# Kernel optimization log

Measured on AMD Instinct MI355X. Metric: run time of the kernel, lower is better.

The kernel has to match this reference:

```python
import jax, jax.numpy as jnp
import numpy as np

N_NODES = 50000
N_EDGES = 500000
D = 128
BN_EPS = 1e-5


def setup_inputs() -> dict:
    key = jax.random.key(0)
    ks = jax.random.split(key, 6)
    x = jax.random.normal(ks[0], (N_NODES, D), dtype=jnp.float32)
    edge_attr = jax.random.normal(ks[1], (N_EDGES, D), dtype=jnp.float32)
    edge_source = jax.random.randint(ks[2], (N_EDGES,), 0, N_NODES, dtype=jnp.int32)
    edge_target = jax.random.randint(ks[3], (N_EDGES,), 0, N_NODES, dtype=jnp.int32)
    # Linear weights stored as [in, out] = [3*D, D]; scaled like torch default init
    scale = 1.0 / np.sqrt(3 * D)
    Wf = jax.random.normal(ks[4], (3 * D, D), dtype=jnp.float32) * scale
    Ws = jax.random.normal(ks[5], (3 * D, D), dtype=jnp.float32) * scale
    bf = jnp.zeros((D,), dtype=jnp.float32)
    bs = jnp.zeros((D,), dtype=jnp.float32)
    gamma = jnp.ones((D,), dtype=jnp.float32)
    beta = jnp.zeros((D,), dtype=jnp.float32)
    return {"x": x, "edge_attr": edge_attr, "edge_source": edge_source,
            "edge_target": edge_target, "Wf": Wf, "bf": bf, "Ws": Ws, "bs": bs,
            "gamma": gamma, "beta": beta}


def reference(x, edge_attr, edge_source, edge_target, Wf, bf, Ws, bs, gamma, beta):
    # gather + concat: z is [E, 3*D]
    z = jnp.concatenate([x[edge_source], x[edge_target], edge_attr], axis=-1)
    # gated edge messages: sigmoid(linear_f(z)) * softplus(linear_s(z))  [E, D]
    msg = jax.nn.sigmoid(z @ Wf + bf) * jax.nn.softplus(z @ Ws + bs)
    # scatter-sum back to source nodes  [N, D]
    agg = jax.ops.segment_sum(msg, edge_source, num_segments=N_NODES)
    # BatchNorm1d (training mode: batch stats, biased variance)
    mean = jnp.mean(agg, axis=0)
    var = jnp.var(agg, axis=0)
    agg_bn = (agg - mean) * jax.lax.rsqrt(var + BN_EPS) * gamma + beta
    return jax.nn.softplus(x + agg_bn)
```

## Files before the change

### kernel.cpp

```cpp
#include <hip/hip_runtime.h>
#include <math.h>
#include <stdint.h>

#define N_NODES 50000
#define N_EDGES 500000
#define D 128
#define BE 128
#define NKT 6
#define WROW 72
#define WSLAB (256 * WROW)
#define MROW 136
#define LOG2E 1.4426950408889634f
#define LN2   0.6931471805599453f

typedef __attribute__((ext_vector_type(8))) short bf16x8;
typedef __attribute__((ext_vector_type(4))) float floatx4;

__device__ __forceinline__ float fast_sigmoid(float v) {
    return __builtin_amdgcn_rcpf(1.0f + __builtin_amdgcn_exp2f(-v * LOG2E));
}
__device__ __forceinline__ float fast_softplus(float v) {
    float t = __builtin_amdgcn_exp2f(-fabsf(v) * LOG2E);
    return fmaxf(v, 0.0f) + __builtin_amdgcn_logf(1.0f + t) * LN2;
}
__device__ __forceinline__ uint32_t pack_bf16(float a, float b) {
    union { float f; uint32_t u; } ca, cb; ca.f = a; cb.f = b;
    return __builtin_amdgcn_perm(cb.u + 0x8000u, ca.u + 0x8000u, 0x07060302);
}
__device__ __forceinline__ unsigned short f2bf(float f) {
    union { float f; uint32_t u; } c; c.f = f;
    return (unsigned short)((c.u + 0x8000u) >> 16);
}

__global__ __launch_bounds__(256) void wt_prepass(
    const float* __restrict__ Wf, const float* __restrict__ Ws,
    unsigned short* __restrict__ Wt)
{
    const int kt = blockIdx.x >> 3;
    const int i  = blockIdx.x & 7;
    const int n  = threadIdx.x;
    const float* src = (n < 128) ? (Wf + n) : (Ws + (n - 128));
    const int k0 = kt * 64 + i * 8;
    uint32_t u[4];
#pragma unroll
    for (int j = 0; j < 4; j++) {
        float a = src[(size_t)(k0 + 2 * j) * D];
        float b = src[(size_t)(k0 + 2 * j + 1) * D];
        u[j] = pack_bf16(a, b);
    }
    uint4 v; v.x = u[0]; v.y = u[1]; v.z = u[2]; v.w = u[3];
    *(uint4*)(Wt + (size_t)(kt * 256 + n) * WROW + i * 8) = v;
}

__global__ __launch_bounds__(512, 2) void edge_msg_mfma(
    const float* __restrict__ x, const float* __restrict__ edge_attr,
    const int* __restrict__ esrc, const int* __restrict__ etgt,
    const unsigned short* __restrict__ Wt,
    const float* __restrict__ bfp, const float* __restrict__ bsp,
    float* __restrict__ agg, unsigned short* __restrict__ msgs,
    int* __restrict__ cnt, int mode)
{
    __shared__ unsigned short sW[2 * WSLAB];
    __shared__ unsigned short sZ[BE * WROW];
    __shared__ int sSrc[BE];
    __shared__ int sTgt[BE];

    const int tid  = threadIdx.x;
    const int lane = tid & 63;
    const int w    = tid >> 6;
    const int wc   = w & 3;
    const int wr   = w >> 2;
    const int e0   = blockIdx.x * BE;

    if (tid < BE) {
        sSrc[tid] = (e0 + tid < N_EDGES) ? esrc[e0 + tid] : 0;
    } else if (tid < 2 * BE) {
        int m = tid - BE;
        sTgt[m] = (e0 + m < N_EDGES) ? etgt[e0 + m] : 0;
    }
    __syncthreads();

    floatx4 acc[4][4];
#pragma unroll
    for (int mt = 0; mt < 4; mt++)
#pragma unroll
        for (int nt = 0; nt < 4; nt++) {
            floatx4 z = {0.f, 0.f, 0.f, 0.f};
            acc[mt][nt] = z;
        }

    const int zm = tid >> 2;
    const int zk = (tid & 3) * 16;

    float4 zr0, zr1, zr2, zr3;

    auto issue_w = [&](int kt, int slab) {
        const char* gbase = (const char*)Wt + (size_t)kt * 36864 + lane * 16;
        char* lbase = (char*)sW + slab * 36864;
#pragma unroll
        for (int i = 0; i < 5; i++) {
            int c = w + i * 8;
            if (c < 36) {
                __builtin_amdgcn_global_load_lds(
                    (const __attribute__((address_space(1))) void*)(gbase + c * 1024),
                    (__attribute__((address_space(3))) void*)(lbase + c * 1024),
                    16, 0, 0);
            }
        }
    };
    auto issue_z = [&](int kt) {
        const float* zsrc;
        int half = (kt & 1) * 64;
        if (kt < 2)      zsrc = x + (size_t)sSrc[zm] * D + half;
        else if (kt < 4) zsrc = x + (size_t)sTgt[zm] * D + half;
        else {
            int eg = e0 + zm;
            zsrc = edge_attr + (size_t)(eg < N_EDGES ? eg : 0) * D + half;
        }
        zr0 = *(const float4*)(zsrc + zk);
        zr1 = *(const float4*)(zsrc + zk + 4);
        zr2 = *(const float4*)(zsrc + zk + 8);
        zr3 = *(const float4*)(zsrc + zk + 12);
    };

    issue_w(0, 0);
    issue_z(0);

#pragma unroll 1
    for (int kt = 0; kt < NKT; kt++) {
        {
            uint4 lo, hi;
            lo.x = pack_bf16(zr0.x, zr0.y); lo.y = pack_bf16(zr0.z, zr0.w);
            lo.z = pack_bf16(zr1.x, zr1.y); lo.w = pack_bf16(zr1.z, zr1.w);
            hi.x = pack_bf16(zr2.x, zr2.y); hi.y = pack_bf16(zr2.z, zr2.w);
            hi.z = pack_bf16(zr3.x, zr3.y); hi.w = pack_bf16(zr3.z, zr3.w);
            uint32_t* dz = (uint32_t*)(sZ + (size_t)zm * WROW) + (zk >> 1);
            *(uint4*)(dz)     = lo;
            *(uint4*)(dz + 4) = hi;
        }
        __syncthreads();

        if (kt + 1 < NKT) {
            issue_w(kt + 1, (kt + 1) & 1);
            issue_z(kt + 1);
        }

        const unsigned short* sWb = sW + (kt & 1) * WSLAB;
#pragma unroll
        for (int ks = 0; ks < 2; ks++) {
            const int kb = ks * 32 + (lane >> 4) * 8;
            bf16x8 afr[4];
#pragma unroll
            for (int mt = 0; mt < 4; mt++)
                afr[mt] = *(const bf16x8*)(sZ + (wr * 64 + mt * 16 + (lane & 15)) * WROW + kb);
            bf16x8 bfr[4];
#pragma unroll
            for (int nt = 0; nt < 4; nt++) {
                int n = (nt < 2) ? (wc * 32 + nt * 16 + (lane & 15))
                                 : (128 + wc * 32 + (nt - 2) * 16 + (lane & 15));
                bfr[nt] = *(const bf16x8*)(sWb + n * WROW + kb);
            }
#pragma unroll
            for (int mt = 0; mt < 4; mt++)
#pragma unroll
                for (int nt = 0; nt < 4; nt++)
                    acc[mt][nt] = __builtin_amdgcn_mfma_f32_16x16x32_bf16(
                        afr[mt], bfr[nt], acc[mt][nt], 0, 0, 0);
        }
        __builtin_amdgcn_s_barrier();
    }

    if (mode) {
        unsigned short* sM = sW;
#pragma unroll
        for (int nt = 0; nt < 2; nt++) {
            const int col = wc * 32 + nt * 16 + (lane & 15);
            const float bF = bfp[col];
            const float bS = bsp[col];
#pragma unroll
            for (int mt = 0; mt < 4; mt++) {
#pragma unroll
                for (int r = 0; r < 4; r++) {
                    int mm = wr * 64 + mt * 16 + (lane >> 4) * 4 + r;
                    float f = acc[mt][nt][r] + bF;
                    float s = acc[mt][nt + 2][r] + bS;
                    sM[mm * MROW + col] = f2bf(fast_sigmoid(f) * fast_softplus(s));
                }
            }
        }
        __syncthreads();
        {
            const int r = tid >> 2;
            const int c = tid & 3;
            if (e0 + r < N_EDGES) {
                const uint4* sp = (const uint4*)(sM + r * MROW + c * 32);
                uint4 v0 = sp[0], v1 = sp[1], v2 = sp[2], v3 = sp[3];
                uint4* dp = (uint4*)(msgs + (size_t)(e0 + r) * D + c * 32);
                dp[0] = v0; dp[1] = v1; dp[2] = v2; dp[3] = v3;
            }
        }
        if (tid < BE && e0 + tid < N_EDGES) atomicAdd(&cnt[sSrc[tid]], 1);
    } else {
#pragma unroll
        for (int nt = 0; nt < 2; nt++) {
            const int col = wc * 32 + nt * 16 + (lane & 15);
            const float bF = bfp[col];
            const float bS = bsp[col];
#pragma unroll
            for (int mt = 0; mt < 4; mt++) {
#pragma unroll
                for (int r = 0; r < 4; r++) {
                    int mm = wr * 64 + mt * 16 + (lane >> 4) * 4 + r;
                    int eg = e0 + mm;
                    if (eg >= N_EDGES) continue;
                    float f = acc[mt][nt][r] + bF;
                    float s = acc[mt][nt + 2][r] + bS;
                    atomicAdd(agg + (size_t)sSrc[mm] * D + col,
                              fast_sigmoid(f) * fast_softplus(s));
                }
            }
        }
    }
}

__global__ __launch_bounds__(1024) void scan1_kernel(
    const int* __restrict__ cnt, int* __restrict__ ofs, int* __restrict__ bsum)
{
    __shared__ int sh[1024];
    const int t = threadIdx.x;
    const int n = blockIdx.x * 1024 + t;
    int c = (n < N_NODES) ? cnt[n] : 0;
    sh[t] = c;
    __syncthreads();
    for (int off = 1; off < 1024; off <<= 1) {
        int v = (t >= off) ? sh[t - off] : 0;
        __syncthreads();
        sh[t] += v;
        __syncthreads();
    }
    if (n < N_NODES) ofs[n] = sh[t] - c;
    if (t == 1023) bsum[blockIdx.x] = sh[1023];
}

__global__ __launch_bounds__(64) void scan2_kernel(int* __restrict__ bsum)
{
    if (threadIdx.x == 0) {
        int v[49];
#pragma unroll
        for (int i = 0; i < 49; i++) v[i] = bsum[i];
        int run = 0;
#pragma unroll
        for (int i = 0; i < 49; i++) { bsum[i] = run; run += v[i]; }
    }
}

__global__ __launch_bounds__(512) void fill_kernel(
    const int* __restrict__ esrc, int* __restrict__ ofs,
    const int* __restrict__ bsum, int* __restrict__ eidx)
{
    int e = blockIdx.x * 512 + threadIdx.x;
    if (e < N_EDGES) {
        int s = esrc[e];
        int slot = atomicAdd(&ofs[s], 1) + bsum[s >> 10];
        eidx[slot] = e;
    }
}

__global__ __launch_bounds__(256) void gather_kernel(
    const unsigned short* __restrict__ msgs, const int* __restrict__ eidx,
    const int* __restrict__ cnt, const int* __restrict__ ofs,
    const int* __restrict__ bsum, float* __restrict__ agg)
{
    __shared__ float red[2][64][2];
    const int tid  = threadIdx.x;
    const int lane = tid & 63;
    const int w2   = (tid >> 6) & 1;
    const int h    = tid >> 7;
    const int n    = blockIdx.x * 2 + h;
    const int deg  = cnt[n];
    const int base = bsum[n >> 10] + ofs[n] - deg;
    float a0 = 0.0f, a1 = 0.0f;
    for (int j = w2; j < deg; j += 2) {
        int id = eidx[base + j];
        uint32_t p = *(const uint32_t*)(msgs + (size_t)id * D + 2 * lane);
        union { uint32_t u; float f; } c0, c1;
        c0.u = p << 16;
        c1.u = p & 0xFFFF0000u;
        a0 += c0.f; a1 += c1.f;
    }
    if (w2 == 1) { red[h][lane][0] = a0; red[h][lane][1] = a1; }
    __syncthreads();
    if (w2 == 0) {
        a0 += red[h][lane][0];
        a1 += red[h][lane][1];
        float2 o; o.x = a0; o.y = a1;
        *(float2*)(agg + (size_t)n * D + 2 * lane) = o;
    }
}

#define STATS_BLOCKS 128
__global__ __launch_bounds__(256) void bn_stats_kernel(
    const float* __restrict__ agg, float* __restrict__ stats)
{
    __shared__ float4 redS[256];
    __shared__ float4 redQ[256];
    const int c4 = threadIdx.x & 31;
    const int rg = threadIdx.x >> 5;
    const int rows = (N_NODES + STATS_BLOCKS - 1) / STATS_BLOCKS;
    const int r0 = blockIdx.x * rows;
    const int r1 = min(r0 + rows, N_NODES);
    const float4* a4 = (const float4*)agg;

    float4 s = {0, 0, 0, 0}, q = {0, 0, 0, 0};
    for (int r = r0 + rg; r < r1; r += 8) {
        float4 v = a4[(size_t)r * 32 + c4];
        s.x += v.x; s.y += v.y; s.z += v.z; s.w += v.w;
        q.x += v.x * v.x; q.y += v.y * v.y; q.z += v.z * v.z; q.w += v.w * v.w;
    }
    redS[threadIdx.x] = s;
    redQ[threadIdx.x] = q;
    __syncthreads();
    if (rg == 0) {
#pragma unroll
        for (int j = 1; j < 8; j++) {
            float4 ts = redS[c4 + j * 32], tq = redQ[c4 + j * 32];
            s.x += ts.x; s.y += ts.y; s.z += ts.z; s.w += ts.w;
            q.x += tq.x; q.y += tq.y; q.z += tq.z; q.w += tq.w;
        }
        atomicAdd(&stats[c4 * 4 + 0], s.x);
        atomicAdd(&stats[c4 * 4 + 1], s.y);
        atomicAdd(&stats[c4 * 4 + 2], s.z);
        atomicAdd(&stats[c4 * 4 + 3], s.w);
        atomicAdd(&stats[D + c4 * 4 + 0], q.x);
        atomicAdd(&stats[D + c4 * 4 + 1], q.y);
        atomicAdd(&stats[D + c4 * 4 + 2], q.z);
        atomicAdd(&stats[D + c4 * 4 + 3], q.w);
    }
}

__global__ __launch_bounds__(256) void bn_final_kernel(
    const float* __restrict__ x, const float* __restrict__ agg,
    const float* __restrict__ stats,
    const float* __restrict__ gamma, const float* __restrict__ beta,
    float* __restrict__ out)
{
    const int idx = blockIdx.x * blockDim.x + threadIdx.x;
    const int total4 = N_NODES * D / 4;
    if (idx >= total4) return;
    const int c4 = idx & (D / 4 - 1);
    const float inv_n = 1.0f / (float)N_NODES;

    float4 sm = *(const float4*)&stats[c4 * 4];
    float4 sq = *(const float4*)&stats[D + c4 * 4];
    float4 g  = *(const float4*)&gamma[c4 * 4];
    float4 b  = *(const float4*)&beta[c4 * 4];
    float4 xv = ((const float4*)x)[idx];
    float4 av = ((const float4*)agg)[idx];

    float4 o;
    {
        float mean = sm.x * inv_n, var = sq.x * inv_n - mean * mean;
        float is = rsqrtf(var + 1e-5f) * g.x;
        o.x = fast_softplus(xv.x + (av.x - mean) * is + b.x);
    }
    {
        float mean = sm.y * inv_n, var = sq.y * inv_n - mean * mean;
        float is = rsqrtf(var + 1e-5f) * g.y;
        o.y = fast_softplus(xv.y + (av.y - mean) * is + b.y);
    }
    {
        float mean = sm.z * inv_n, var = sq.z * inv_n - mean * mean;
        float is = rsqrtf(var + 1e-5f) * g.z;
        o.z = fast_softplus(xv.z + (av.z - mean) * is + b.z);
    }
    {
        float mean = sm.w * inv_n, var = sq.w * inv_n - mean * mean;
        float is = rsqrtf(var + 1e-5f) * g.w;
        o.w = fast_softplus(xv.w + (av.w - mean) * is + b.w);
    }
    ((float4*)out)[idx] = o;
}

extern "C" void kernel_launch(void* const* d_in, const int* in_sizes, int n_in,
                              void* d_out, int out_size, void* d_ws, size_t ws_size,
                              hipStream_t stream) {
    const float* x         = (const float*)d_in[0];
    const float* edge_attr = (const float*)d_in[1];
    const int*   esrc      = (const int*)d_in[2];
    const int*   etgt      = (const int*)d_in[3];
    const float* Wf        = (const float*)d_in[4];
    const float* bf_       = (const float*)d_in[5];
    const float* Ws        = (const float*)d_in[6];
    const float* bs_       = (const float*)d_in[7];
    const float* gamma     = (const float*)d_in[8];
    const float* beta      = (const float*)d_in[9];
    float* out = (float*)d_out;

    float* agg   = (float*)d_ws;
    float* stats = agg + (size_t)N_NODES * D;
    int*   cnt   = (int*)(stats + 2 * D);
    int*   ofs   = cnt + N_NODES;
    int*   bsum  = ofs + N_NODES;
    unsigned short* Wt = (unsigned short*)(bsum + 256);
    int*   eidx  = (int*)((char*)Wt + 221184);
    unsigned short* msgs = (unsigned short*)(eidx + N_EDGES);
    const size_t NEED = 25600000ULL + 1024 + 200000 + 200000 + 1024
                      + 221184 + 2000000 + 128000000ULL;
    const int mode = (ws_size >= NEED) ? 1 : 0;

    wt_prepass<<<48, 256, 0, stream>>>(Wf, Ws, Wt);
    if (mode) {
        hipMemsetAsync(stats, 0, 1024 + 200000, stream);
        edge_msg_mfma<<<(N_EDGES + BE - 1) / BE, 512, 0, stream>>>(
            x, edge_attr, esrc, etgt, Wt, bf_, bs_, agg, msgs, cnt, 1);
        scan1_kernel<<<49, 1024, 0, stream>>>(cnt, ofs, bsum);
        scan2_kernel<<<1, 64, 0, stream>>>(bsum);
        fill_kernel<<<(N_EDGES + 511) / 512, 512, 0, stream>>>(esrc, ofs, bsum, eidx);
        gather_kernel<<<N_NODES / 2, 256, 0, stream>>>(msgs, eidx, cnt, ofs, bsum, agg);
    } else {
        hipMemsetAsync(d_ws, 0, ((size_t)N_NODES * D + 2 * D) * sizeof(float), stream);
        edge_msg_mfma<<<(N_EDGES + BE - 1) / BE, 512, 0, stream>>>(
            x, edge_attr, esrc, etgt, Wt, bf_, bs_, agg, msgs, cnt, 0);
    }
    bn_stats_kernel<<<STATS_BLOCKS, 256, 0, stream>>>(agg, stats);
    bn_final_kernel<<<(N_NODES * D / 4 + 255) / 256, 256, 0, stream>>>(
        x, agg, stats, gamma, beta, out);
}
```

Measured before the change: 730.1 us.

## Split weight slabs into half-K stages and double-buffer Z tile

```diff
diff --git a/kernel.cpp b/kernel.cpp
--- a/kernel.cpp
+++ b/kernel.cpp
@@ -8,7 +8,9 @@
 #define BE 128
 #define NKT 6
 #define WROW 72
-#define WSLAB (256 * WROW)
+#define ZSLAB (BE * WROW)
+#define WKROW 40
+#define WKSLAB (256 * WKROW)
 #define MROW 136
 #define LOG2E 1.4426950408889634f
 #define LN2   0.6931471805599453f
@@ -41,6 +43,8 @@
     const int n  = threadIdx.x;
     const float* src = (n < 128) ? (Wf + n) : (Ws + (n - 128));
     const int k0 = kt * 64 + i * 8;
+    const int s  = kt * 2 + (i >> 2);
+    const int kq = (i & 3) * 8;
     uint32_t u[4];
 #pragma unroll
     for (int j = 0; j < 4; j++) {
@@ -49,7 +53,7 @@
         u[j] = pack_bf16(a, b);
     }
     uint4 v; v.x = u[0]; v.y = u[1]; v.z = u[2]; v.w = u[3];
-    *(uint4*)(Wt + (size_t)(kt * 256 + n) * WROW + i * 8) = v;
+    *(uint4*)(Wt + (size_t)(s * 256 + n) * WKROW + kq) = v;
 }
 
 __global__ __launch_bounds__(512, 2) void edge_msg_mfma(
@@ -60,8 +64,8 @@
     float* __restrict__ agg, unsigned short* __restrict__ msgs,
     int* __restrict__ cnt, int mode)
 {
-    __shared__ unsigned short sW[2 * WSLAB];
-    __shared__ unsigned short sZ[BE * WROW];
+    __shared__ unsigned short sW[2 * WKSLAB];
+    __shared__ unsigned short sZ[2 * ZSLAB];
     __shared__ int sSrc[BE];
     __shared__ int sTgt[BE];
 
@@ -94,13 +98,13 @@
 
     float4 zr0, zr1, zr2, zr3;
 
-    auto issue_w = [&](int kt, int slab) {
-        const char* gbase = (const char*)Wt + (size_t)kt * 36864 + lane * 16;
-        char* lbase = (char*)sW + slab * 36864;
-#pragma unroll
-        for (int i = 0; i < 5; i++) {
+    auto issue_w = [&](int s) {
+        const char* gbase = (const char*)Wt + (size_t)s * 20480 + lane * 16;
+        char* lbase = (char*)sW + (s & 1) * 20480;
+#pragma unroll
+        for (int i = 0; i < 3; i++) {
             int c = w + i * 8;
-            if (c < 36) {
+            if (c < 20) {
                 __builtin_amdgcn_global_load_lds(
                     (const __attribute__((address_space(1))) void*)(gbase + c * 1024),
                     (__attribute__((address_space(3))) void*)(lbase + c * 1024),
@@ -122,9 +126,32 @@
         zr2 = *(const float4*)(zsrc + zk + 8);
         zr3 = *(const float4*)(zsrc + zk + 12);
     };
-
-    issue_w(0, 0);
+    auto compute_stage = [&](int kt, int ks) {
+        const unsigned short* sZb = sZ + (kt & 1) * ZSLAB;
+        const unsigned short* sWb = sW + ((2 * kt + ks) & 1) * WKSLAB;
+        const int kb  = ks * 32 + (lane >> 4) * 8;
+        const int kwb = (lane >> 4) * 8;
+        bf16x8 afr[4];
+#pragma unroll
+        for (int mt = 0; mt < 4; mt++)
+            afr[mt] = *(const bf16x8*)(sZb + (wr * 64 + mt * 16 + (lane & 15)) * WROW + kb);
+        bf16x8 bfr[4];
+#pragma unroll
+        for (int nt = 0; nt < 4; nt++) {
+            int n = (nt < 2) ? (wc * 32 + nt * 16 + (lane & 15))
+                             : (128 + wc * 32 + (nt - 2) * 16 + (lane & 15));
+            bfr[nt] = *(const bf16x8*)(sWb + n * WKROW + kwb);
+        }
+#pragma unroll
+        for (int mt = 0; mt < 4; mt++)
+#pragma unroll
+            for (int nt = 0; nt < 4; nt++)
+                acc[mt][nt] = __builtin_amdgcn_mfma_f32_16x16x32_bf16(
+                    afr[mt], bfr[nt], acc[mt][nt], 0, 0, 0);
+    };
+
     issue_z(0);
+    issue_w(0);
 
 #pragma unroll 1
     for (int kt = 0; kt < NKT; kt++) {
@@ -134,44 +161,24 @@
             lo.z = pack_bf16(zr1.x, zr1.y); lo.w = pack_bf16(zr1.z, zr1.w);
             hi.x = pack_bf16(zr2.x, zr2.y); hi.y = pack_bf16(zr2.z, zr2.w);
             hi.z = pack_bf16(zr3.x, zr3.y); hi.w = pack_bf16(zr3.z, zr3.w);
-            uint32_t* dz = (uint32_t*)(sZ + (size_t)zm * WROW) + (zk >> 1);
+            uint32_t* dz = (uint32_t*)(sZ + (kt & 1) * ZSLAB + (size_t)zm * WROW) + (zk >> 1);
             *(uint4*)(dz)     = lo;
             *(uint4*)(dz + 4) = hi;
         }
         __syncthreads();
-
+        issue_w(2 * kt + 1);
+        compute_stage(kt, 0);
+        __syncthreads();
         if (kt + 1 < NKT) {
-            issue_w(kt + 1, (kt + 1) & 1);
             issue_z(kt + 1);
-        }
-
-        const unsigned short* sWb = sW + (kt & 1) * WSLAB;
-#pragma unroll
-        for (int ks = 0; ks < 2; ks++) {
-            const int kb = ks * 32 + (lane >> 4) * 8;
-            bf16x8 afr[4];
-#pragma unroll
-            for (int mt = 0; mt < 4; mt++)
-                afr[mt] = *(const bf16x8*)(sZ + (wr * 64 + mt * 16 + (lane & 15)) * WROW + kb);
-            bf16x8 bfr[4];
-#pragma unroll
-            for (int nt = 0; nt < 4; nt++) {
-                int n = (nt < 2) ? (wc * 32 + nt * 16 + (lane & 15))
-                                 : (128 + wc * 32 + (nt - 2) * 16 + (lane & 15));
-                bfr[nt] = *(const bf16x8*)(sWb + n * WROW + kb);
-            }
-#pragma unroll
-            for (int mt = 0; mt < 4; mt++)
-#pragma unroll
-                for (int nt = 0; nt < 4; nt++)
-                    acc[mt][nt] = __builtin_amdgcn_mfma_f32_16x16x32_bf16(
-                        afr[mt], bfr[nt], acc[mt][nt], 0, 0, 0);
-        }
-        __builtin_amdgcn_s_barrier();
+            issue_w(2 * kt + 2);
+        }
+        compute_stage(kt, 1);
     }
 
     if (mode) {
         unsigned short* sM = sW;
+        __syncthreads();
 #pragma unroll
         for (int nt = 0; nt < 2; nt++) {
             const int col = wc * 32 + nt * 16 + (lane & 15);
@@ -402,10 +409,10 @@
     int*   ofs   = cnt + N_NODES;
     int*   bsum  = ofs + N_NODES;
     unsigned short* Wt = (unsigned short*)(bsum + 256);
-    int*   eidx  = (int*)((char*)Wt + 221184);
+    int*   eidx  = (int*)((char*)Wt + 245760);
     unsigned short* msgs = (unsigned short*)(eidx + N_EDGES);
     const size_t NEED = 25600000ULL + 1024 + 200000 + 200000 + 1024
-                      + 221184 + 2000000 + 128000000ULL;
+                      + 245760 + 2000000 + 128000000ULL;
     const int mode = (ws_size >= NEED) ? 1 : 0;
 
     wt_prepass<<<48, 256, 0, stream>>>(Wf, Ws, Wt);
```

Measured after the change: 660.8 us. -9.5%, faster.
